# Kernel tuning notes

Hardware: AMD Instinct MI355X
Metric: run time of the kernel (lower is better)

## Reference

```python
import math
import jax, jax.numpy as jnp
import numpy as np

B, T, H = 4096, 49, 512

def setup_inputs() -> dict:
    key = jax.random.key(0)
    ks = jax.random.split(key, 13)
    sc = 1.0 / math.sqrt(H)
    return {
        "v": jax.random.normal(ks[0], (B, T, H), dtype=jnp.float32),
        "h": jax.random.normal(ks[1], (B, H), dtype=jnp.float32),
        "s": jax.random.normal(ks[2], (B, H), dtype=jnp.float32),
        "W_h": jax.random.normal(ks[3], (H, H), dtype=jnp.float32) * sc,
        "b_h": jax.random.normal(ks[4], (H,), dtype=jnp.float32) * sc,
        "W_v": jax.random.normal(ks[5], (H, H), dtype=jnp.float32) * sc,
        "b_v": jax.random.normal(ks[6], (H,), dtype=jnp.float32) * sc,
        "w_z": jax.random.normal(ks[7], (H,), dtype=jnp.float32) * sc,
        "b_z": jax.random.normal(ks[8], (), dtype=jnp.float32) * sc,
        "W_s": jax.random.normal(ks[9], (H, H), dtype=jnp.float32) * sc,
        "b_s": jax.random.normal(ks[10], (H,), dtype=jnp.float32) * sc,
        "w_beta": jax.random.normal(ks[11], (H,), dtype=jnp.float32) * sc,
        "b_beta": jax.random.normal(ks[12], (), dtype=jnp.float32) * sc,
    }

def reference(v, h, s, W_h, b_h, W_v, b_v, w_z, b_z, W_s, b_s, w_beta, b_beta):
    # eval mode: dropout is identity
    h_proj = h @ W_h + b_h                                  # [B, H]
    v_proj = jnp.einsum('bth,hk->btk', v, W_v) + b_v        # [B, T, H]
    z = jnp.tanh(h_proj[:, None, :] + v_proj)               # [B, T, H]
    z = jnp.einsum('bth,h->bt', z, w_z) + b_z               # [B, T]
    beta = jnp.tanh((s @ W_s + b_s + h_proj) * math.sqrt(0.5))  # [B, H]
    beta = (beta @ w_beta + b_beta)[:, None]                # [B, 1]
    a = jax.nn.softmax(jnp.concatenate([z, beta], axis=1), axis=1)  # [B, T+1]
    v_ext = jnp.concatenate([v, s[:, None, :]], axis=1)     # [B, T+1, H]
    c = jnp.einsum('bt,bth->bh', a, v_ext)                  # [B, H]
    return c
```

## Files before the change

kernel.cpp:

```cpp
#include <hip/hip_runtime.h>
#include <stdint.h>

#define B_ 4096
#define T_ 49
#define H_ 512
#define BT_ (B_*T_)
#define BB 16

typedef __bf16 bf16x8 __attribute__((ext_vector_type(8)));
typedef float  f32x4  __attribute__((ext_vector_type(4)));
typedef unsigned short ushort_;

__device__ __forceinline__ ushort_ f2bf(float f){
  unsigned int u = __float_as_uint(f);
  u += 0x7fffu + ((u >> 16) & 1u);
  return (ushort_)(u >> 16);
}

__device__ __forceinline__ float fast_tanh(float x){
  float e = __expf(2.0f * x);
  return 1.0f - 2.0f * __builtin_amdgcn_rcpf(e + 1.0f);
}

__global__ __launch_bounds__(256) void k_pack(const float* __restrict__ W,
                                              ushort_* __restrict__ pack){
  int idx = blockIdx.x * 256 + threadIdx.x;
  int lane = idx & 63;
  int gt   = (idx >> 6) & 31;
  int kk   = idx >> 11;
  int col  = gt*16 + (lane & 15);
  int k0   = kk*32 + (lane >> 4)*8;
  ushort4 lo, hi;
  lo.x = f2bf(W[(k0+0)*H_ + col]);
  lo.y = f2bf(W[(k0+1)*H_ + col]);
  lo.z = f2bf(W[(k0+2)*H_ + col]);
  lo.w = f2bf(W[(k0+3)*H_ + col]);
  hi.x = f2bf(W[(k0+4)*H_ + col]);
  hi.y = f2bf(W[(k0+5)*H_ + col]);
  hi.z = f2bf(W[(k0+6)*H_ + col]);
  hi.w = f2bf(W[(k0+7)*H_ + col]);
  ushort4* dst = (ushort4*)pack;
  dst[idx*2]   = lo;
  dst[idx*2+1] = hi;
}

__global__ __launch_bounds__(256) void k_proj2(
    const float* __restrict__ h, const float* __restrict__ s,
    const ushort_* __restrict__ whp, const ushort_* __restrict__ wsp,
    const float* __restrict__ bh, const float* __restrict__ bs,
    const float* __restrict__ bv, const float* __restrict__ wbeta,
    const float* __restrict__ bbeta_p,
    float* __restrict__ hpb, float* __restrict__ beta)
{
  __shared__ __align__(16) ushort_ hl[16*H_];
  __shared__ __align__(16) ushort_ sl[16*H_];
  __shared__ float zwp[4][16];
  const int tid = threadIdx.x;
  const int w = tid >> 6, lane = tid & 63;
  const int l15 = lane & 15, l4 = lane >> 4;
  const int b0 = blockIdx.x * 16;

  {
    const int r = tid >> 4;
    const float4* hsrc = (const float4*)(h + (size_t)(b0+r)*H_);
    const float4* ssrc = (const float4*)(s + (size_t)(b0+r)*H_);
    #pragma unroll
    for(int p=0;p<8;p++){
      int q  = (tid & 15) + p*16;
      int k0 = q*4;
      float4 fh = hsrc[q];
      float4 fs = ssrc[q];
      int idx = (k0>>5)*512 + ((((k0&31)>>3)<<4) + r)*8 + (k0&7);
      ushort4 uh; uh.x=f2bf(fh.x); uh.y=f2bf(fh.y); uh.z=f2bf(fh.z); uh.w=f2bf(fh.w);
      ushort4 us; us.x=f2bf(fs.x); us.y=f2bf(fs.y); us.z=f2bf(fs.z); us.w=f2bf(fs.w);
      *(ushort4*)&hl[idx] = uh;
      *(ushort4*)&sl[idx] = us;
    }
  }
  __syncthreads();

  const bf16x8* __restrict__ bph = (const bf16x8*)whp;
  const bf16x8* __restrict__ bps = (const bf16x8*)wsp;
  const int bbase = w*512 + lane;

  f32x4 acch[8], accs[8];
  #pragma unroll
  for(int ni=0;ni<8;ni++){ acch[ni]=(f32x4){0,0,0,0}; accs[ni]=(f32x4){0,0,0,0}; }

  #pragma unroll 2
  for(int kk=0;kk<16;kk++){
    bf16x8 ah = *(const bf16x8*)&hl[kk*512 + lane*8];
    bf16x8 as2 = *(const bf16x8*)&sl[kk*512 + lane*8];
    #pragma unroll
    for(int ni=0;ni<8;ni++){
      acch[ni] = __builtin_amdgcn_mfma_f32_16x16x32_bf16(ah,  bph[kk*2048 + bbase + ni*64], acch[ni], 0,0,0);
      accs[ni] = __builtin_amdgcn_mfma_f32_16x16x32_bf16(as2, bps[kk*2048 + bbase + ni*64], accs[ni], 0,0,0);
    }
  }

  float bhv[8], bsv[8], bvv[8], wbv[8];
  #pragma unroll
  for(int ni=0;ni<8;ni++){
    int col = w*128 + ni*16 + l15;
    bhv[ni] = bh[col]; bsv[ni] = bs[col]; bvv[ni] = bv[col]; wbv[ni] = wbeta[col];
  }
  float btsum[4];
  #pragma unroll
  for(int rr=0;rr<4;rr++){
    int row = l4*4 + rr;
    float bsum = 0.f;
    #pragma unroll
    for(int ni=0;ni<8;ni++){
      int col = w*128 + ni*16 + l15;
      float hp = acch[ni][rr] + bhv[ni];
      hpb[(size_t)(b0+row)*H_ + col] = hp + bvv[ni];
      float bt = fast_tanh((accs[ni][rr] + bsv[ni] + hp) * 0.70710678118654752f);
      bsum = fmaf(bt, wbv[ni], bsum);
    }
    btsum[rr] = bsum;
  }
  #pragma unroll
  for(int rr=0;rr<4;rr++){
    btsum[rr] += __shfl_xor(btsum[rr], 1);
    btsum[rr] += __shfl_xor(btsum[rr], 2);
    btsum[rr] += __shfl_xor(btsum[rr], 4);
    btsum[rr] += __shfl_xor(btsum[rr], 8);
    if(l15 == 0) zwp[w][l4*4+rr] = btsum[rr];
  }
  __syncthreads();
  if(tid < 16)
    beta[b0+tid] = zwp[0][tid] + zwp[1][tid] + zwp[2][tid] + zwp[3][tid] + bbeta_p[0];
}

__global__ __launch_bounds__(256, 3) void k_fused(
    const float* __restrict__ v, const ushort_* __restrict__ bpack,
    const float* __restrict__ hpb, const float* __restrict__ wz,
    const float* __restrict__ bz_p, const float* __restrict__ beta,
    const float* __restrict__ s, float* __restrict__ out)
{
  __shared__ __align__(16) ushort_ Av[49*512];
  __shared__ float zw[4][64];
  __shared__ float a_s[64];
  const int tid = threadIdx.x;
  const int w = tid >> 6, lane = tid & 63;
  const int l15 = lane & 15, l4 = lane >> 4;
  const int b = blockIdx.x;

  const f32x4* __restrict__ vsrc = (const f32x4*)(v + (size_t)b * T_ * H_);
  const bf16x8* __restrict__ bp = (const bf16x8*)bpack;
  const int bbase = w*256 + lane;

  const int srow = tid >> 4, c4 = tid & 15;
  const int slot = ((c4 >> 1) ^ (srow & 7));
  const int wsub = ((c4 & 1) << 3);
  const bool r48 = (tid < 16);

#define VLOAD(N0,N1,N2,N3, CH) { \
    N0 = __builtin_nontemporal_load(vsrc + (srow     )*128 + (CH)*16 + c4); \
    N1 = __builtin_nontemporal_load(vsrc + (srow + 16)*128 + (CH)*16 + c4); \
    N2 = __builtin_nontemporal_load(vsrc + (srow + 32)*128 + (CH)*16 + c4); \
    if(r48) N3 = __builtin_nontemporal_load(vsrc + 48*128 + (CH)*16 + c4); }

#define SWRITE(N0,N1,N2,N3, CH) { \
    const int cb_ = (CH)*128; ushort4 u_; \
    u_.x=f2bf(N0[0]); u_.y=f2bf(N0[1]); u_.z=f2bf(N0[2]); u_.w=f2bf(N0[3]); \
    *(ushort4*)((char*)Av + (srow   )*1024 + cb_ + (slot<<4) + wsub) = u_; \
    u_.x=f2bf(N1[0]); u_.y=f2bf(N1[1]); u_.z=f2bf(N1[2]); u_.w=f2bf(N1[3]); \
    *(ushort4*)((char*)Av + (srow+16)*1024 + cb_ + (slot<<4) + wsub) = u_; \
    u_.x=f2bf(N2[0]); u_.y=f2bf(N2[1]); u_.z=f2bf(N2[2]); u_.w=f2bf(N2[3]); \
    *(ushort4*)((char*)Av + (srow+32)*1024 + cb_ + (slot<<4) + wsub) = u_; \
    if(r48){ \
      u_.x=f2bf(N3[0]); u_.y=f2bf(N3[1]); u_.z=f2bf(N3[2]); u_.w=f2bf(N3[3]); \
      *(ushort4*)((char*)Av + 48*1024 + cb_ + (slot<<4) + wsub) = u_; } }

#define AFRAG(af, KS) { \
    _Pragma("unroll") \
    for(int mi=0;mi<4;mi++){ \
      int row_ = (mi < 3) ? (mi*16 + l15) : 48; \
      int g_   = ((KS)*4 + l4) ^ (row_ & 7); \
      af[mi] = *(const bf16x8*)((const char*)Av + row_*1024 + (g_<<4)); } }

#define MFMA16(af, bfr) { \
    __builtin_amdgcn_s_setprio(1); \
    _Pragma("unroll") \
    for(int mi=0;mi<4;mi++) \
      _Pragma("unroll") \
      for(int ni=0;ni<4;ni++) \
        acc[mi][ni] = __builtin_amdgcn_mfma_f32_16x16x32_bf16(af[mi], bfr[ni], acc[mi][ni], 0,0,0); \
    __builtin_amdgcn_s_setprio(0); }

  {
    f32x4 A0,A1,A2,A3, B0,B1,B2,B3;
    VLOAD(A0,A1,A2,A3, 0)
    #pragma unroll
    for(int cc=0; cc<4; cc++){
      VLOAD(B0,B1,B2,B3, 2*cc+1)
      SWRITE(A0,A1,A2,A3, 2*cc)
      if(cc < 3) VLOAD(A0,A1,A2,A3, 2*cc+2)
      SWRITE(B0,B1,B2,B3, 2*cc+1)
    }
  }

  f32x4 acc[4][4];
  #pragma unroll
  for(int mi=0;mi<4;mi++)
    #pragma unroll
    for(int ni=0;ni<4;ni++) acc[mi][ni] = (f32x4){0.f,0.f,0.f,0.f};

  bf16x8 ba[4], bb[4], af[4];
  #pragma unroll
  for(int ni=0;ni<4;ni++) ba[ni] = bp[bbase + ni*64];
  __syncthreads();

  #pragma unroll 1
  for(int kk=0; kk<16; kk+=2){
    #pragma unroll
    for(int ni=0;ni<4;ni++) bb[ni] = bp[(kk+1)*2048 + bbase + ni*64];
    AFRAG(af, kk)
    MFMA16(af, ba)
    if(kk < 14){
      #pragma unroll
      for(int ni=0;ni<4;ni++) ba[ni] = bp[(kk+2)*2048 + bbase + ni*64];
    }
    AFRAG(af, kk+1)
    MFMA16(af, bb)
  }

  {
    float wzv[4], hp0[4];
    #pragma unroll
    for(int ni=0;ni<4;ni++){
      int col = w*64 + ni*16 + l15;
      wzv[ni] = wz[col];
      hp0[ni] = hpb[(size_t)b*H_ + col];
    }
    float zp[16];
    #pragma unroll
    for(int mi=0;mi<4;mi++)
      #pragma unroll
      for(int r=0;r<4;r++){
        float az = 0.f;
        #pragma unroll
        for(int ni=0;ni<4;ni++)
          az = fmaf(fast_tanh(acc[mi][ni][r] + hp0[ni]), wzv[ni], az);
        zp[mi*4+r] = az;
      }
    #pragma unroll
    for(int i=0;i<16;i++){
      zp[i] += __shfl_xor(zp[i], 1);
      zp[i] += __shfl_xor(zp[i], 2);
      zp[i] += __shfl_xor(zp[i], 4);
      zp[i] += __shfl_xor(zp[i], 8);
    }
    if(l15 == 0){
      #pragma unroll
      for(int mi=0;mi<4;mi++)
        #pragma unroll
        for(int r=0;r<4;r++)
          zw[w][mi*16 + l4*4 + r] = zp[mi*4+r];
    }
  }

  #pragma unroll
  for(int mi=0;mi<4;mi++)
    #pragma unroll
    for(int ni=0;ni<4;ni++) acc[mi][ni] = (f32x4){0.f,0.f,0.f,0.f};

  #pragma unroll
  for(int ni=0;ni<4;ni++) ba[ni] = bp[1024 + bbase + ni*64];

  #pragma unroll 1
  for(int kk=0; kk<16; kk+=2){
    #pragma unroll
    for(int ni=0;ni<4;ni++) bb[ni] = bp[(kk+1)*2048 + 1024 + bbase + ni*64];
    AFRAG(af, kk)
    MFMA16(af, ba)
    if(kk < 14){
      #pragma unroll
      for(int ni=0;ni<4;ni++) ba[ni] = bp[(kk+2)*2048 + 1024 + bbase + ni*64];
    }
    AFRAG(af, kk+1)
    MFMA16(af, bb)
  }

  {
    float wzv[4], hp0[4];
    #pragma unroll
    for(int ni=0;ni<4;ni++){
      int col = 256 + w*64 + ni*16 + l15;
      wzv[ni] = wz[col];
      hp0[ni] = hpb[(size_t)b*H_ + col];
    }
    float zp[16];
    #pragma unroll
    for(int mi=0;mi<4;mi++)
      #pragma unroll
      for(int r=0;r<4;r++){
        float az = 0.f;
        #pragma unroll
        for(int ni=0;ni<4;ni++)
          az = fmaf(fast_tanh(acc[mi][ni][r] + hp0[ni]), wzv[ni], az);
        zp[mi*4+r] = az;
      }
    #pragma unroll
    for(int i=0;i<16;i++){
      zp[i] += __shfl_xor(zp[i], 1);
      zp[i] += __shfl_xor(zp[i], 2);
      zp[i] += __shfl_xor(zp[i], 4);
      zp[i] += __shfl_xor(zp[i], 8);
    }
    if(l15 == 0){
      #pragma unroll
      for(int mi=0;mi<4;mi++)
        #pragma unroll
        for(int r=0;r<4;r++)
          zw[w][mi*16 + l4*4 + r] += zp[mi*4+r];
    }
  }
  __syncthreads();

  if(tid < 64){
    float zv;
    if(tid < T_)       zv = zw[0][tid] + zw[1][tid] + zw[2][tid] + zw[3][tid] + bz_p[0];
    else if(tid == T_) zv = beta[b];
    else               zv = -3.0e38f;
    float m = zv;
    #pragma unroll
    for(int off=32;off>=1;off>>=1) m = fmaxf(m, __shfl_xor(m, off));
    float e = (tid <= T_) ? __expf(zv - m) : 0.f;
    float ssum = e;
    #pragma unroll
    for(int off=32;off>=1;off>>=1) ssum += __shfl_xor(ssum, off);
    a_s[tid] = e * __builtin_amdgcn_rcpf(ssum);
  }
  __syncthreads();

  const int n0 = tid * 2;
  float ax = 0.f, ay = 0.f;
  #pragma unroll 7
  for(int t=0;t<T_;t++){
    float at = a_s[t];
    unsigned int u = *(const unsigned int*)((const char*)Av + t*1024
                       + ((((n0>>3) ^ (t&7)))<<4) + ((n0&7)<<1));
    float x = __uint_as_float((u & 0xFFFFu) << 16);
    float y = __uint_as_float(u & 0xFFFF0000u);
    ax = fmaf(at, x, ax);
    ay = fmaf(at, y, ay);
  }
  float a49 = a_s[T_];
  float2 sv = ((const float2*)(s + (size_t)b*H_))[tid];
  ax = fmaf(a49, sv.x, ax);
  ay = fmaf(a49, sv.y, ay);
  float2 res; res.x = ax; res.y = ay;
  ((float2*)(out + (size_t)b*H_))[tid] = res;
}

extern "C" void kernel_launch(void* const* d_in, const int* in_sizes, int n_in,
                              void* d_out, int out_size, void* d_ws, size_t ws_size,
                              hipStream_t stream)
{
  const float* v   = (const float*)d_in[0];
  const float* h   = (const float*)d_in[1];
  const float* s   = (const float*)d_in[2];
  const float* Wh  = (const float*)d_in[3];
  const float* bh  = (const float*)d_in[4];
  const float* Wv  = (const float*)d_in[5];
  const float* bv  = (const float*)d_in[6];
  const float* wz  = (const float*)d_in[7];
  const float* bz  = (const float*)d_in[8];
  const float* Ws  = (const float*)d_in[9];
  const float* bs  = (const float*)d_in[10];
  const float* wb  = (const float*)d_in[11];
  const float* bbet= (const float*)d_in[12];
  float* out = (float*)d_out;

  float* hpb  = (float*)d_ws;
  float* beta = hpb + (size_t)B_*H_;
  ushort_* bpack = (ushort_*)(beta + B_);
  ushort_* whp   = bpack + (size_t)H_*H_;
  ushort_* wsp   = whp   + (size_t)H_*H_;

  k_pack <<<128, 256, 0, stream>>>(Wv, bpack);
  k_pack <<<128, 256, 0, stream>>>(Wh, whp);
  k_pack <<<128, 256, 0, stream>>>(Ws, wsp);
  k_proj2<<<B_/16, 256, 0, stream>>>(h, s, whp, wsp, bh, bs, bv, wb, bbet, hpb, beta);
  k_fused<<<B_, 256, 0, stream>>>(v, bpack, hpb, wz, bz, beta, s, out);
}
```

Measured before the change: 218.0 us.

## Deepen B-fragment prefetch, double-buffer A fragments, merge pack kernels

The two MFMA loops in the fused kernel are fully unrolled. They now keep a 4-deep ring of B-weight fragments in flight from global memory and double-buffer the A fragments read from LDS, so load latency overlaps with MFMA issue. The extra registers this needs are covered by relaxing the launch bound's minimum blocks per SM from 3 to 2. The three weight-pack launches are merged into one 384-block kernel to cut launch overhead. The cost is lower occupancy and more register pressure in the main kernel.

```diff
diff --git a/kernel.cpp b/kernel.cpp
--- a/kernel.cpp
+++ b/kernel.cpp
@@ -5,7 +5,6 @@
 #define T_ 49
 #define H_ 512
 #define BT_ (B_*T_)
-#define BB 16
 
 typedef __bf16 bf16x8 __attribute__((ext_vector_type(8)));
 typedef float  f32x4  __attribute__((ext_vector_type(4)));
@@ -16,15 +15,22 @@
   u += 0x7fffu + ((u >> 16) & 1u);
   return (ushort_)(u >> 16);
 }
-
+__device__ __forceinline__ float bf2f(ushort_ u){
+  return __uint_as_float(((unsigned int)u) << 16);
+}
 __device__ __forceinline__ float fast_tanh(float x){
   float e = __expf(2.0f * x);
   return 1.0f - 2.0f * __builtin_amdgcn_rcpf(e + 1.0f);
 }
 
-__global__ __launch_bounds__(256) void k_pack(const float* __restrict__ W,
-                                              ushort_* __restrict__ pack){
-  int idx = blockIdx.x * 256 + threadIdx.x;
+__global__ __launch_bounds__(256) void k_pack3(
+    const float* __restrict__ Wv, const float* __restrict__ Wh,
+    const float* __restrict__ Ws, ushort_* __restrict__ bpack,
+    ushort_* __restrict__ whp, ushort_* __restrict__ wsp){
+  const int grp = blockIdx.x >> 7;
+  const float* W = (grp==0) ? Wv : (grp==1) ? Wh : Ws;
+  ushort_* pack  = (grp==0) ? bpack : (grp==1) ? whp : wsp;
+  int idx = (blockIdx.x & 127) * 256 + threadIdx.x;
   int lane = idx & 63;
   int gt   = (idx >> 6) & 31;
   int kk   = idx >> 11;
@@ -132,13 +138,13 @@
     beta[b0+tid] = zwp[0][tid] + zwp[1][tid] + zwp[2][tid] + zwp[3][tid] + bbeta_p[0];
 }
 
-__global__ __launch_bounds__(256, 3) void k_fused(
+__global__ __launch_bounds__(256, 2) void k_fused(
     const float* __restrict__ v, const ushort_* __restrict__ bpack,
     const float* __restrict__ hpb, const float* __restrict__ wz,
     const float* __restrict__ bz_p, const float* __restrict__ beta,
     const float* __restrict__ s, float* __restrict__ out)
 {
-  __shared__ __align__(16) ushort_ Av[49*512];
+  __shared__ __align__(16) ushort_ Av[T_*H_];
   __shared__ float zw[4][64];
   __shared__ float a_s[64];
   const int tid = threadIdx.x;
@@ -202,28 +208,30 @@
   }
 
   f32x4 acc[4][4];
+  bf16x8 bq[4][4];
+  bf16x8 af2[2][4];
+
   #pragma unroll
   for(int mi=0;mi<4;mi++)
     #pragma unroll
     for(int ni=0;ni<4;ni++) acc[mi][ni] = (f32x4){0.f,0.f,0.f,0.f};
 
-  bf16x8 ba[4], bb[4], af[4];
-  #pragma unroll
-  for(int ni=0;ni<4;ni++) ba[ni] = bp[bbase + ni*64];
-  __syncthreads();
-
-  #pragma unroll 1
-  for(int kk=0; kk<16; kk+=2){
-    #pragma unroll
-    for(int ni=0;ni<4;ni++) bb[ni] = bp[(kk+1)*2048 + bbase + ni*64];
-    AFRAG(af, kk)
-    MFMA16(af, ba)
-    if(kk < 14){
-      #pragma unroll
-      for(int ni=0;ni<4;ni++) ba[ni] = bp[(kk+2)*2048 + bbase + ni*64];
-    }
-    AFRAG(af, kk+1)
-    MFMA16(af, bb)
+  #pragma unroll
+  for(int p=0;p<4;p++)
+    #pragma unroll
+    for(int ni=0;ni<4;ni++) bq[p][ni] = bp[p*2048 + bbase + ni*64];
+
+  __syncthreads();
+
+  AFRAG(af2[0], 0)
+  #pragma unroll
+  for(int kk=0; kk<16; kk++){
+    if(kk < 15){ AFRAG(af2[(kk+1)&1], kk+1) }
+    MFMA16(af2[kk&1], bq[kk&3])
+    if(kk < 12){
+      #pragma unroll
+      for(int ni=0;ni<4;ni++) bq[kk&3][ni] = bp[(kk+4)*2048 + bbase + ni*64];
+    }
   }
 
   {
@@ -267,20 +275,19 @@
     for(int ni=0;ni<4;ni++) acc[mi][ni] = (f32x4){0.f,0.f,0.f,0.f};
 
   #pragma unroll
-  for(int ni=0;ni<4;ni++) ba[ni] = bp[1024 + bbase + ni*64];
-
-  #pragma unroll 1
-  for(int kk=0; kk<16; kk+=2){
-    #pragma unroll
-    for(int ni=0;ni<4;ni++) bb[ni] = bp[(kk+1)*2048 + 1024 + bbase + ni*64];
-    AFRAG(af, kk)
-    MFMA16(af, ba)
-    if(kk < 14){
-      #pragma unroll
-      for(int ni=0;ni<4;ni++) ba[ni] = bp[(kk+2)*2048 + 1024 + bbase + ni*64];
-    }
-    AFRAG(af, kk+1)
-    MFMA16(af, bb)
+  for(int p=0;p<4;p++)
+    #pragma unroll
+    for(int ni=0;ni<4;ni++) bq[p][ni] = bp[p*2048 + 1024 + bbase + ni*64];
+
+  AFRAG(af2[0], 0)
+  #pragma unroll
+  for(int kk=0; kk<16; kk++){
+    if(kk < 15){ AFRAG(af2[(kk+1)&1], kk+1) }
+    MFMA16(af2[kk&1], bq[kk&3])
+    if(kk < 12){
+      #pragma unroll
+      for(int ni=0;ni<4;ni++) bq[kk&3][ni] = bp[(kk+4)*2048 + 1024 + bbase + ni*64];
+    }
   }
 
   {
@@ -380,9 +387,7 @@
   ushort_* whp   = bpack + (size_t)H_*H_;
   ushort_* wsp   = whp   + (size_t)H_*H_;
 
-  k_pack <<<128, 256, 0, stream>>>(Wv, bpack);
-  k_pack <<<128, 256, 0, stream>>>(Wh, whp);
-  k_pack <<<128, 256, 0, stream>>>(Ws, wsp);
+  k_pack3<<<384, 256, 0, stream>>>(Wv, Wh, Ws, bpack, whp, wsp);
   k_proj2<<<B_/16, 256, 0, stream>>>(h, s, whp, wsp, bh, bs, bv, wb, bbet, hpb, beta);
   k_fused<<<B_, 256, 0, stream>>>(v, bpack, hpb, wz, bz, beta, s, out);
 }
```

New measurement: 220.3 us. Within noise of the previous version (+1.1%).
